# Optimization experiments

Measured on AMD Instinct MI355X. Metric: run time of the kernel, lower is better.

The kernel has to match this reference:

```python
import jax, jax.numpy as jnp
import numpy as np

N = 150000
E = 1200000
IN_DIM = 64
HID = 64


def setup_inputs() -> dict:
    key = jax.random.key(0)
    k1, k2, k3, k4 = jax.random.split(key, 4)
    obs = jax.random.normal(k1, (N, IN_DIM), dtype=jnp.float32)
    edge_index = jax.random.randint(k2, (2, E), 0, N, dtype=jnp.int64)
    # GCNConv layer params (Glorot-style scale)
    W1 = jax.random.normal(k3, (IN_DIM, HID), dtype=jnp.float32) / jnp.sqrt(IN_DIM)
    b1 = jnp.zeros((HID,), dtype=jnp.float32)
    W2 = jax.random.normal(k4, (HID, 1), dtype=jnp.float32) / jnp.sqrt(HID)
    b2 = jnp.zeros((1,), dtype=jnp.float32)
    return {"obs": obs, "edge_index": edge_index, "W1": W1, "b1": b1, "W2": W2, "b2": b2}


def gcn_conv(x, W, b, src, dst, n):
    # PyG GCNConv: x' = D^{-1/2} (A + I) D^{-1/2} (x W) + b
    x = x @ W  # [N, F_out]
    # degree with self-loops (edge weight 1)
    deg = jax.ops.segment_sum(jnp.ones((src.shape[0],), x.dtype), dst, num_segments=n) + 1.0
    dinv = jax.lax.rsqrt(deg)  # deg >= 1, safe
    norm = dinv[src] * dinv[dst]  # per-edge norm
    msg = x[src] * norm[:, None]  # gather + scale
    agg = jax.ops.segment_sum(msg, dst, num_segments=n)
    agg = agg + x * (dinv * dinv)[:, None]  # self-loop term
    return agg + b


def reference(obs, edge_index, W1, b1, W2, b2):
    src, dst = edge_index[0], edge_index[1]
    h1 = jax.nn.relu(gcn_conv(obs, W1, b1, src, dst, N))
    h2 = jax.nn.relu(gcn_conv(h1, W2, b2, src, dst, N))
    out = h2.reshape(-1, 15)[:, 3:].reshape(-1)
    return out
```

## Files before the change

kernel.cpp:

```cpp
#include <hip/hip_runtime.h>
#include <hip/hip_bf16.h>


#define BK 256
#define NBMAX 640
#define EPB 4096
#define HB 320
#define FCAP 3072

typedef unsigned int uint;
typedef unsigned short ushort;
typedef __attribute__((ext_vector_type(8))) short bf16x8_t;
typedef __attribute__((ext_vector_type(4))) float f32x4_t;

static __device__ __forceinline__ ushort f2bf(float x) {
    uint u = __float_as_uint(x);
    u = (u + 0x7FFFu + ((u >> 16) & 1u)) >> 16;
    return (ushort)u;
}

static __device__ __forceinline__ uint pk2(float a, float b) {
    __hip_bfloat162 h = __float22bfloat162_rn(make_float2(a, b));
    return *(uint*)&h;
}

__global__ __launch_bounds__(256) void k_hist(const int* __restrict__ dst, int E, int nb,
                                              int* __restrict__ hist) {
    __shared__ int h[NBMAX];
    const int t = threadIdx.x, b = blockIdx.x;
    for (int j = t; j < nb; j += 256) h[j] = 0;
    __syncthreads();
    const int e0 = b * EPB, e1 = min(e0 + EPB, E);
    if ((((size_t)dst) & 15) == 0) {
        const int nfull = (e1 - e0) & ~3;
        const int4* d4 = (const int4*)(dst + e0);
        for (int i = t; i < (nfull >> 2); i += 256) {
            int4 d = d4[i];
            atomicAdd(&h[d.x >> 8], 1); atomicAdd(&h[d.y >> 8], 1);
            atomicAdd(&h[d.z >> 8], 1); atomicAdd(&h[d.w >> 8], 1);
        }
        for (int e = e0 + nfull + t; e < e1; e += 256) atomicAdd(&h[dst[e] >> 8], 1);
    } else {
        for (int e = e0 + t; e < e1; e += 256) atomicAdd(&h[dst[e] >> 8], 1);
    }
    __syncthreads();
    for (int j = t; j < nb; j += 256) hist[j * HB + b] = h[j];
}

__global__ __launch_bounds__(256) void k_cscan1(int* __restrict__ hist, int nblk,
                                                int* __restrict__ colsum) {
    __shared__ int s[256];
    const int j = blockIdx.x, t = threadIdx.x;
    int carry = 0;
    for (int base = 0; base < nblk; base += 256) {
        int idx = base + t;
        int v = (idx < nblk) ? hist[j * HB + idx] : 0;
        __syncthreads();
        s[t] = v;
        __syncthreads();
        for (int o = 1; o < 256; o <<= 1) {
            int x = s[t];
            if (t >= o) x += s[t - o];
            __syncthreads();
            s[t] = x;
            __syncthreads();
        }
        if (idx < nblk) hist[j * HB + idx] = carry + s[t] - v;
        carry += s[255];
    }
    if (t == 0) colsum[j] = carry;
}

__global__ __launch_bounds__(1024) void k_cscan2(const int* __restrict__ colsum, int nb, int N,
                                                 int* __restrict__ boff, int* __restrict__ rowptr) {
    __shared__ int s[1024];
    const int t = threadIdx.x;
    int v = (t < nb) ? colsum[t] : 0;
    s[t] = v;
    __syncthreads();
    for (int o = 1; o < 1024; o <<= 1) {
        int x = s[t];
        if (t >= o) x += s[t - o];
        __syncthreads();
        s[t] = x;
        __syncthreads();
    }
    if (t < nb) boff[t] = s[t] - v;
    if (t == nb - 1) { boff[nb] = s[t]; rowptr[N] = s[t]; }
}

__global__ __launch_bounds__(256) void k_place(const int* __restrict__ src, const int* __restrict__ dst,
                                               int E, int nb, const int* __restrict__ hist,
                                               const int* __restrict__ boff, uint* __restrict__ ebuf) {
    __shared__ int cur[NBMAX];
    const int t = threadIdx.x, b = blockIdx.x;
    for (int j = t; j < nb; j += 256) cur[j] = boff[j] + hist[j * HB + b];
    __syncthreads();
    const int e0 = b * EPB, e1 = min(e0 + EPB, E);
    if (((((size_t)dst) | ((size_t)src)) & 15) == 0) {
        const int nfull = (e1 - e0) & ~3;
        const int4* d4 = (const int4*)(dst + e0);
        const int4* s4 = (const int4*)(src + e0);
        for (int i = t; i < (nfull >> 2); i += 256) {
            int4 d = d4[i];
            int4 s = s4[i];
            int p;
            p = atomicAdd(&cur[d.x >> 8], 1); ebuf[p] = ((uint)(d.x & 255) << 24) | (uint)s.x;
            p = atomicAdd(&cur[d.y >> 8], 1); ebuf[p] = ((uint)(d.y & 255) << 24) | (uint)s.y;
            p = atomicAdd(&cur[d.z >> 8], 1); ebuf[p] = ((uint)(d.z & 255) << 24) | (uint)s.z;
            p = atomicAdd(&cur[d.w >> 8], 1); ebuf[p] = ((uint)(d.w & 255) << 24) | (uint)s.w;
        }
        for (int e = e0 + nfull + t; e < e1; e += 256) {
            int d = dst[e];
            int p = atomicAdd(&cur[d >> 8], 1);
            ebuf[p] = ((uint)(d & 255) << 24) | (uint)src[e];
        }
    } else {
        for (int e = e0 + t; e < e1; e += 256) {
            int d = dst[e];
            int p = atomicAdd(&cur[d >> 8], 1);
            ebuf[p] = ((uint)(d & 255) << 24) | (uint)src[e];
        }
    }
}

__global__ __launch_bounds__(256) void k_fill3(const uint* __restrict__ ebuf, const int* __restrict__ boff,
                                               int N, int* __restrict__ rowptr, float* __restrict__ dinv,
                                               int* __restrict__ csrc) {
    __shared__ int cnt[BK];
    __shared__ int sc[BK];
    __shared__ int cur[BK];
    __shared__ uint se[FCAP];
    const int b = blockIdx.x, v0 = b << 8, t = threadIdx.x;
    const int nv = min(BK, N - v0);
    cnt[t] = 0;
    __syncthreads();
    const int bb = boff[b], be = boff[b + 1];
    const int ne = be - bb;
    for (int j = t; j < ne; j += 256) {
        uint e = ebuf[bb + j];
        if (j < FCAP) se[j] = e;
        atomicAdd(&cnt[e >> 24], 1);
    }
    __syncthreads();
    const int c = cnt[t];
    if (t < nv) dinv[v0 + t] = rsqrtf((float)c + 1.0f);
    sc[t] = c;
    __syncthreads();
    for (int o = 1; o < 256; o <<= 1) {
        int x = sc[t];
        if (t >= o) x += sc[t - o];
        __syncthreads();
        sc[t] = x;
        __syncthreads();
    }
    const int ex = sc[t] - c + bb;
    if (t < nv) rowptr[v0 + t] = ex;
    cur[t] = ex;
    __syncthreads();
    for (int j = t; j < ne; j += 256) {
        uint e = (j < FCAP) ? se[j] : ebuf[bb + j];
        int p = atomicAdd(&cur[e >> 24], 1);
        csrc[p] = (int)(e & 0xFFFFFFu);
    }
}

__global__ __launch_bounds__(256) void k_gemm1(const float* __restrict__ X, const float* __restrict__ W,
                                               const float* __restrict__ dinv, int N,
                                               ushort* __restrict__ Yh) {
    __shared__ __align__(16) ushort Wt[64 * 72];
    __shared__ __align__(16) ushort Ot[64 * 72];
    const int t = threadIdx.x;

#pragma unroll
    for (int i = 0; i < 4; i++) {
        int idx = t + i * 256;
        int k = idx >> 4;
        int c4 = idx & 15;
        float4 w4 = ((const float4*)W)[idx];
        Wt[(c4 * 4 + 0) * 72 + k] = f2bf(w4.x);
        Wt[(c4 * 4 + 1) * 72 + k] = f2bf(w4.y);
        Wt[(c4 * 4 + 2) * 72 + k] = f2bf(w4.z);
        Wt[(c4 * 4 + 3) * 72 + k] = f2bf(w4.w);
    }
    __syncthreads();

    const int l = t & 63;
    const int lr = l & 15;
    const int g = l >> 4;
    const int wv = t >> 6;

#pragma unroll
    for (int tile = 0; tile < 2; tile++) {
        const int row0 = blockIdx.x * 128 + tile * 64;
        const int rw = row0 + wv * 16;

        bf16x8_t afr[2];
#pragma unroll
        for (int s = 0; s < 2; s++) {
            const int row = rw + lr;
            float4 xa = make_float4(0.f, 0.f, 0.f, 0.f), xb = xa;
            if (row < N) {
                const float4* xp = (const float4*)(X + (size_t)row * 64 + s * 32 + g * 8);
                xa = xp[0];
                xb = xp[1];
            }
            uint4 ua;
            ua.x = pk2(xa.x, xa.y);
            ua.y = pk2(xa.z, xa.w);
            ua.z = pk2(xb.x, xb.y);
            ua.w = pk2(xb.z, xb.w);
            afr[s] = __builtin_bit_cast(bf16x8_t, ua);
        }

        const float4 dv = *(const float4*)(dinv + rw + g * 4);

#pragma unroll
        for (int c = 0; c < 4; c++) {
            f32x4_t acc = {0.f, 0.f, 0.f, 0.f};
#pragma unroll
            for (int s = 0; s < 2; s++) {
                const bf16x8_t bf = *(const bf16x8_t*)&Wt[(c * 16 + lr) * 72 + s * 32 + g * 8];
                acc = __builtin_amdgcn_mfma_f32_16x16x32_bf16(afr[s], bf, acc, 0, 0, 0);
            }
            const int col = c * 16 + lr;
            const int rb = wv * 16 + g * 4;
            uint u01 = pk2(acc[0] * dv.x, acc[1] * dv.y);
            uint u23 = pk2(acc[2] * dv.z, acc[3] * dv.w);
            Ot[(rb + 0) * 72 + col] = (ushort)(u01 & 0xFFFFu);
            Ot[(rb + 1) * 72 + col] = (ushort)(u01 >> 16);
            Ot[(rb + 2) * 72 + col] = (ushort)(u23 & 0xFFFFu);
            Ot[(rb + 3) * 72 + col] = (ushort)(u23 >> 16);
        }
        __syncthreads();

#pragma unroll
        for (int i = 0; i < 2; i++) {
            int vi = t + i * 256;
            int row = vi >> 3;
            int c8 = vi & 7;
            int grow = row0 + row;
            if (grow < N)
                ((uint4*)(Yh + (size_t)grow * 64))[c8] = *(const uint4*)&Ot[row * 72 + c8 * 8];
        }
        __syncthreads();
    }
}

__global__ __launch_bounds__(256) void k_agg(const ushort* __restrict__ Yh, const int* __restrict__ rowptr,
                                             const int* __restrict__ csrc, const float* __restrict__ dinv,
                                             const float* __restrict__ b1, const float* __restrict__ W2,
                                             int N, float* __restrict__ zs) {
    int t = blockIdx.x * 256 + threadIdx.x;
    int v = t >> 3;
    if (v >= N) return;
    int li = t & 7;
    const uint4* Y4 = (const uint4*)Yh;
    int start = rowptr[v];
    int cnt = rowptr[v + 1] - start;

    float a[8];
    {
        uint4 m = Y4[(size_t)v * 8 + li];
        a[0] = __uint_as_float(m.x << 16);
        a[1] = __uint_as_float(m.x & 0xFFFF0000u);
        a[2] = __uint_as_float(m.y << 16);
        a[3] = __uint_as_float(m.y & 0xFFFF0000u);
        a[4] = __uint_as_float(m.z << 16);
        a[5] = __uint_as_float(m.z & 0xFFFF0000u);
        a[6] = __uint_as_float(m.w << 16);
        a[7] = __uint_as_float(m.w & 0xFFFF0000u);
    }

    int idx = (li < cnt) ? csrc[start + li] : 0;
    for (int j0 = 0; j0 < cnt; j0 += 8) {
        int rem = cnt - j0;
        int nxt = 0;
        if (li < rem - 8) nxt = csrc[start + j0 + 8 + li];
#pragma unroll
        for (int k = 0; k < 8; k++) {
            if (k < rem) {
                int s = __shfl(idx, k, 8);
                uint4 m = Y4[(size_t)s * 8 + li];
                a[0] += __uint_as_float(m.x << 16);
                a[1] += __uint_as_float(m.x & 0xFFFF0000u);
                a[2] += __uint_as_float(m.y << 16);
                a[3] += __uint_as_float(m.y & 0xFFFF0000u);
                a[4] += __uint_as_float(m.z << 16);
                a[5] += __uint_as_float(m.z & 0xFFFF0000u);
                a[6] += __uint_as_float(m.w << 16);
                a[7] += __uint_as_float(m.w & 0xFFFF0000u);
            }
        }
        idx = nxt;
    }

    float dv = dinv[v];
    float4 ba = ((const float4*)b1)[2 * li], bb = ((const float4*)b1)[2 * li + 1];
    float4 wa = ((const float4*)W2)[2 * li], wb = ((const float4*)W2)[2 * li + 1];
    float p;
    p  = fmaxf(fmaf(dv, a[0], ba.x), 0.f) * wa.x;
    p += fmaxf(fmaf(dv, a[1], ba.y), 0.f) * wa.y;
    p += fmaxf(fmaf(dv, a[2], ba.z), 0.f) * wa.z;
    p += fmaxf(fmaf(dv, a[3], ba.w), 0.f) * wa.w;
    p += fmaxf(fmaf(dv, a[4], bb.x), 0.f) * wb.x;
    p += fmaxf(fmaf(dv, a[5], bb.y), 0.f) * wb.y;
    p += fmaxf(fmaf(dv, a[6], bb.z), 0.f) * wb.z;
    p += fmaxf(fmaf(dv, a[7], bb.w), 0.f) * wb.w;
    p += __shfl_xor(p, 1);
    p += __shfl_xor(p, 2);
    p += __shfl_xor(p, 4);
    if (li == 0) zs[v] = p * dv;
}

__global__ __launch_bounds__(256) void k_out2(const float* __restrict__ zs, const int* __restrict__ rowptr,
                                              const int* __restrict__ csrc, const float* __restrict__ dinv,
                                              const float* __restrict__ b2, int M, float* __restrict__ out) {
    int i = blockIdx.x * 256 + threadIdx.x;
    if (i >= M) return;
    int q = i / 12;
    int c = i - q * 12;
    int v = q * 15 + 3 + c;
    int j = rowptr[v];
    const int end = rowptr[v + 1];
    float s = zs[v];
    for (; j + 4 <= end; j += 4) {
        int i0 = csrc[j], i1 = csrc[j + 1], i2 = csrc[j + 2], i3 = csrc[j + 3];
        s += zs[i0] + zs[i1] + zs[i2] + zs[i3];
    }
    for (; j < end; j++) s += zs[csrc[j]];
    out[i] = fmaxf(fmaf(dinv[v], s, b2[0]), 0.f);
}

extern "C" void kernel_launch(void* const* d_in, const int* in_sizes, int n_in,
                              void* d_out, int out_size, void* d_ws, size_t ws_size,
                              hipStream_t stream) {
    const float* obs = (const float*)d_in[0];
    const int*   ei  = (const int*)d_in[1];
    const float* W1  = (const float*)d_in[2];
    const float* b1  = (const float*)d_in[3];
    const float* W2  = (const float*)d_in[4];
    const float* b2  = (const float*)d_in[5];

    const int N = in_sizes[0] / 64;
    const int E = in_sizes[1] / 2;
    const int M = out_size;
    const int NB = (N + BK - 1) / BK;
    const int NBLK = (E + EPB - 1) / EPB;

    const int* src = ei;
    const int* dst = ei + E;

    ushort* Yh     = (ushort*)d_ws;
    float*  dinv   = (float*)(Yh + (size_t)N * 64);
    float*  zs     = dinv + N;
    int*    rowptr = (int*)(zs + N);
    int*    colsum = rowptr + N + 1;
    int*    boff   = colsum + NBMAX;
    int*    hist   = boff + NBMAX + 1;
    uint*   ebuf   = (uint*)(hist + NBMAX * HB);
    int*    csrc   = (int*)(ebuf + E);

    k_hist  <<<NBLK, 256, 0, stream>>>(dst, E, NB, hist);
    k_cscan1<<<NB, 256, 0, stream>>>(hist, NBLK, colsum);
    k_cscan2<<<1, 1024, 0, stream>>>(colsum, NB, N, boff, rowptr);
    k_place <<<NBLK, 256, 0, stream>>>(src, dst, E, NB, hist, boff, ebuf);
    k_fill3 <<<NB, 256, 0, stream>>>(ebuf, boff, N, rowptr, dinv, csrc);
    k_gemm1 <<<(N + 127) / 128, 256, 0, stream>>>(obs, W1, dinv, N, Yh);
    k_agg   <<<((size_t)N * 8 + 255) / 256, 256, 0, stream>>>(Yh, rowptr, csrc, dinv, b1, W2, N, zs);
    k_out2  <<<(M + 255) / 256, 256, 0, stream>>>(zs, rowptr, csrc, dinv, b2, M, (float*)d_out);
}
```

Baseline: 89.42 us.

## Fuse histogram with GEMM, drop column-scan kernel, move dinv scaling into aggregation

The destination histogram and the first-layer GEMM now run in one launch, split by block index. This works because the GEMM no longer pre-scales rows by dinv. The source-side dinv factor is applied instead inside the aggregation loop, with a per-neighbour dinv gather and an FMA. The single-block k_cscan2 is removed: k_place rescans colsum itself and k_fill3 reduces a colsum prefix, cutting two launches and one serial step. The cost is extra dinv gathers per edge in aggregation and redundant scan work in every place/fill block.

Measured after the change: 90.00 us. About the same (+0.6%).

```diff
diff --git a/kernel.cpp b/kernel.cpp
--- a/kernel.cpp
+++ b/kernel.cpp
@@ -24,153 +24,38 @@
     return *(uint*)&h;
 }
 
-__global__ __launch_bounds__(256) void k_hist(const int* __restrict__ dst, int E, int nb,
-                                              int* __restrict__ hist) {
-    __shared__ int h[NBMAX];
-    const int t = threadIdx.x, b = blockIdx.x;
-    for (int j = t; j < nb; j += 256) h[j] = 0;
-    __syncthreads();
-    const int e0 = b * EPB, e1 = min(e0 + EPB, E);
-    if ((((size_t)dst) & 15) == 0) {
-        const int nfull = (e1 - e0) & ~3;
-        const int4* d4 = (const int4*)(dst + e0);
-        for (int i = t; i < (nfull >> 2); i += 256) {
-            int4 d = d4[i];
-            atomicAdd(&h[d.x >> 8], 1); atomicAdd(&h[d.y >> 8], 1);
-            atomicAdd(&h[d.z >> 8], 1); atomicAdd(&h[d.w >> 8], 1);
-        }
-        for (int e = e0 + nfull + t; e < e1; e += 256) atomicAdd(&h[dst[e] >> 8], 1);
-    } else {
-        for (int e = e0 + t; e < e1; e += 256) atomicAdd(&h[dst[e] >> 8], 1);
-    }
-    __syncthreads();
-    for (int j = t; j < nb; j += 256) hist[j * HB + b] = h[j];
-}
-
-__global__ __launch_bounds__(256) void k_cscan1(int* __restrict__ hist, int nblk,
-                                                int* __restrict__ colsum) {
-    __shared__ int s[256];
-    const int j = blockIdx.x, t = threadIdx.x;
-    int carry = 0;
-    for (int base = 0; base < nblk; base += 256) {
-        int idx = base + t;
-        int v = (idx < nblk) ? hist[j * HB + idx] : 0;
-        __syncthreads();
-        s[t] = v;
-        __syncthreads();
-        for (int o = 1; o < 256; o <<= 1) {
-            int x = s[t];
-            if (t >= o) x += s[t - o];
-            __syncthreads();
-            s[t] = x;
-            __syncthreads();
-        }
-        if (idx < nblk) hist[j * HB + idx] = carry + s[t] - v;
-        carry += s[255];
-    }
-    if (t == 0) colsum[j] = carry;
-}
-
-__global__ __launch_bounds__(1024) void k_cscan2(const int* __restrict__ colsum, int nb, int N,
-                                                 int* __restrict__ boff, int* __restrict__ rowptr) {
-    __shared__ int s[1024];
+__global__ __launch_bounds__(256) void k_hist_gemm(const int* __restrict__ dst, int E, int nb, int nblk,
+                                                   int* __restrict__ hist,
+                                                   const float* __restrict__ X, const float* __restrict__ W,
+                                                   int N, ushort* __restrict__ Yh) {
+    __shared__ __align__(16) ushort smem[64 * 72 * 2];
     const int t = threadIdx.x;
-    int v = (t < nb) ? colsum[t] : 0;
-    s[t] = v;
-    __syncthreads();
-    for (int o = 1; o < 1024; o <<= 1) {
-        int x = s[t];
-        if (t >= o) x += s[t - o];
-        __syncthreads();
-        s[t] = x;
-        __syncthreads();
-    }
-    if (t < nb) boff[t] = s[t] - v;
-    if (t == nb - 1) { boff[nb] = s[t]; rowptr[N] = s[t]; }
-}
-
-__global__ __launch_bounds__(256) void k_place(const int* __restrict__ src, const int* __restrict__ dst,
-                                               int E, int nb, const int* __restrict__ hist,
-                                               const int* __restrict__ boff, uint* __restrict__ ebuf) {
-    __shared__ int cur[NBMAX];
-    const int t = threadIdx.x, b = blockIdx.x;
-    for (int j = t; j < nb; j += 256) cur[j] = boff[j] + hist[j * HB + b];
-    __syncthreads();
-    const int e0 = b * EPB, e1 = min(e0 + EPB, E);
-    if (((((size_t)dst) | ((size_t)src)) & 15) == 0) {
-        const int nfull = (e1 - e0) & ~3;
-        const int4* d4 = (const int4*)(dst + e0);
-        const int4* s4 = (const int4*)(src + e0);
-        for (int i = t; i < (nfull >> 2); i += 256) {
-            int4 d = d4[i];
-            int4 s = s4[i];
-            int p;
-            p = atomicAdd(&cur[d.x >> 8], 1); ebuf[p] = ((uint)(d.x & 255) << 24) | (uint)s.x;
-            p = atomicAdd(&cur[d.y >> 8], 1); ebuf[p] = ((uint)(d.y & 255) << 24) | (uint)s.y;
-            p = atomicAdd(&cur[d.z >> 8], 1); ebuf[p] = ((uint)(d.z & 255) << 24) | (uint)s.z;
-            p = atomicAdd(&cur[d.w >> 8], 1); ebuf[p] = ((uint)(d.w & 255) << 24) | (uint)s.w;
-        }
-        for (int e = e0 + nfull + t; e < e1; e += 256) {
-            int d = dst[e];
-            int p = atomicAdd(&cur[d >> 8], 1);
-            ebuf[p] = ((uint)(d & 255) << 24) | (uint)src[e];
-        }
-    } else {
-        for (int e = e0 + t; e < e1; e += 256) {
-            int d = dst[e];
-            int p = atomicAdd(&cur[d >> 8], 1);
-            ebuf[p] = ((uint)(d & 255) << 24) | (uint)src[e];
-        }
-    }
-}
-
-__global__ __launch_bounds__(256) void k_fill3(const uint* __restrict__ ebuf, const int* __restrict__ boff,
-                                               int N, int* __restrict__ rowptr, float* __restrict__ dinv,
-                                               int* __restrict__ csrc) {
-    __shared__ int cnt[BK];
-    __shared__ int sc[BK];
-    __shared__ int cur[BK];
-    __shared__ uint se[FCAP];
-    const int b = blockIdx.x, v0 = b << 8, t = threadIdx.x;
-    const int nv = min(BK, N - v0);
-    cnt[t] = 0;
-    __syncthreads();
-    const int bb = boff[b], be = boff[b + 1];
-    const int ne = be - bb;
-    for (int j = t; j < ne; j += 256) {
-        uint e = ebuf[bb + j];
-        if (j < FCAP) se[j] = e;
-        atomicAdd(&cnt[e >> 24], 1);
-    }
-    __syncthreads();
-    const int c = cnt[t];
-    if (t < nv) dinv[v0 + t] = rsqrtf((float)c + 1.0f);
-    sc[t] = c;
-    __syncthreads();
-    for (int o = 1; o < 256; o <<= 1) {
-        int x = sc[t];
-        if (t >= o) x += sc[t - o];
-        __syncthreads();
-        sc[t] = x;
-        __syncthreads();
-    }
-    const int ex = sc[t] - c + bb;
-    if (t < nv) rowptr[v0 + t] = ex;
-    cur[t] = ex;
-    __syncthreads();
-    for (int j = t; j < ne; j += 256) {
-        uint e = (j < FCAP) ? se[j] : ebuf[bb + j];
-        int p = atomicAdd(&cur[e >> 24], 1);
-        csrc[p] = (int)(e & 0xFFFFFFu);
-    }
-}
-
-__global__ __launch_bounds__(256) void k_gemm1(const float* __restrict__ X, const float* __restrict__ W,
-                                               const float* __restrict__ dinv, int N,
-                                               ushort* __restrict__ Yh) {
-    __shared__ __align__(16) ushort Wt[64 * 72];
-    __shared__ __align__(16) ushort Ot[64 * 72];
-    const int t = threadIdx.x;
+
+    if (blockIdx.x < (uint)nblk) {
+        int* h = (int*)smem;
+        const int b = blockIdx.x;
+        for (int j = t; j < nb; j += 256) h[j] = 0;
+        __syncthreads();
+        const int e0 = b * EPB, e1 = min(e0 + EPB, E);
+        if ((((size_t)dst) & 15) == 0) {
+            const int nfull = (e1 - e0) & ~3;
+            const int4* d4 = (const int4*)(dst + e0);
+            for (int i = t; i < (nfull >> 2); i += 256) {
+                int4 d = d4[i];
+                atomicAdd(&h[d.x >> 8], 1); atomicAdd(&h[d.y >> 8], 1);
+                atomicAdd(&h[d.z >> 8], 1); atomicAdd(&h[d.w >> 8], 1);
+            }
+            for (int e = e0 + nfull + t; e < e1; e += 256) atomicAdd(&h[dst[e] >> 8], 1);
+        } else {
+            for (int e = e0 + t; e < e1; e += 256) atomicAdd(&h[dst[e] >> 8], 1);
+        }
+        __syncthreads();
+        for (int j = t; j < nb; j += 256) hist[j * HB + b] = h[j];
+        return;
+    }
+
+    ushort* Wt = smem;
+    ushort* Ot = smem + 64 * 72;
 
 #pragma unroll
     for (int i = 0; i < 4; i++) {
@@ -189,10 +74,11 @@
     const int lr = l & 15;
     const int g = l >> 4;
     const int wv = t >> 6;
+    const int gb = blockIdx.x - nblk;
 
 #pragma unroll
     for (int tile = 0; tile < 2; tile++) {
-        const int row0 = blockIdx.x * 128 + tile * 64;
+        const int row0 = gb * 128 + tile * 64;
         const int rw = row0 + wv * 16;
 
         bf16x8_t afr[2];
@@ -213,8 +99,6 @@
             afr[s] = __builtin_bit_cast(bf16x8_t, ua);
         }
 
-        const float4 dv = *(const float4*)(dinv + rw + g * 4);
-
 #pragma unroll
         for (int c = 0; c < 4; c++) {
             f32x4_t acc = {0.f, 0.f, 0.f, 0.f};
@@ -225,8 +109,8 @@
             }
             const int col = c * 16 + lr;
             const int rb = wv * 16 + g * 4;
-            uint u01 = pk2(acc[0] * dv.x, acc[1] * dv.y);
-            uint u23 = pk2(acc[2] * dv.z, acc[3] * dv.w);
+            uint u01 = pk2(acc[0], acc[1]);
+            uint u23 = pk2(acc[2], acc[3]);
             Ot[(rb + 0) * 72 + col] = (ushort)(u01 & 0xFFFFu);
             Ot[(rb + 1) * 72 + col] = (ushort)(u01 >> 16);
             Ot[(rb + 2) * 72 + col] = (ushort)(u23 & 0xFFFFu);
@@ -244,6 +128,136 @@
                 ((uint4*)(Yh + (size_t)grow * 64))[c8] = *(const uint4*)&Ot[row * 72 + c8 * 8];
         }
         __syncthreads();
+    }
+}
+
+__global__ __launch_bounds__(256) void k_cscan1(int* __restrict__ hist, int nblk,
+                                                int* __restrict__ colsum) {
+    __shared__ int s[256];
+    const int j = blockIdx.x, t = threadIdx.x;
+    int carry = 0;
+    for (int base = 0; base < nblk; base += 256) {
+        int idx = base + t;
+        int v = (idx < nblk) ? hist[j * HB + idx] : 0;
+        __syncthreads();
+        s[t] = v;
+        __syncthreads();
+        for (int o = 1; o < 256; o <<= 1) {
+            int x = s[t];
+            if (t >= o) x += s[t - o];
+            __syncthreads();
+            s[t] = x;
+            __syncthreads();
+        }
+        if (idx < nblk) hist[j * HB + idx] = carry + s[t] - v;
+        carry += s[255];
+    }
+    if (t == 0) colsum[j] = carry;
+}
+
+__global__ __launch_bounds__(256) void k_place(const int* __restrict__ src, const int* __restrict__ dst,
+                                               int E, int nb, const int* __restrict__ hist,
+                                               const int* __restrict__ colsum, uint* __restrict__ ebuf) {
+    __shared__ int cur[NBMAX];
+    __shared__ int s[256];
+    const int t = threadIdx.x, b = blockIdx.x;
+
+    int carry = 0;
+    for (int base = 0; base < nb; base += 256) {
+        int idx = base + t;
+        int v = (idx < nb) ? colsum[idx] : 0;
+        __syncthreads();
+        s[t] = v;
+        __syncthreads();
+        for (int o = 1; o < 256; o <<= 1) {
+            int x = s[t];
+            if (t >= o) x += s[t - o];
+            __syncthreads();
+            s[t] = x;
+            __syncthreads();
+        }
+        if (idx < nb) cur[idx] = carry + s[t] - v + hist[idx * HB + b];
+        carry += s[255];
+    }
+    __syncthreads();
+
+    const int e0 = b * EPB, e1 = min(e0 + EPB, E);
+    if (((((size_t)dst) | ((size_t)src)) & 15) == 0) {
+        const int nfull = (e1 - e0) & ~3;
+        const int4* d4 = (const int4*)(dst + e0);
+        const int4* s4 = (const int4*)(src + e0);
+        for (int i = t; i < (nfull >> 2); i += 256) {
+            int4 d = d4[i];
+            int4 sv = s4[i];
+            int p;
+            p = atomicAdd(&cur[d.x >> 8], 1); ebuf[p] = ((uint)(d.x & 255) << 24) | (uint)sv.x;
+            p = atomicAdd(&cur[d.y >> 8], 1); ebuf[p] = ((uint)(d.y & 255) << 24) | (uint)sv.y;
+            p = atomicAdd(&cur[d.z >> 8], 1); ebuf[p] = ((uint)(d.z & 255) << 24) | (uint)sv.z;
+            p = atomicAdd(&cur[d.w >> 8], 1); ebuf[p] = ((uint)(d.w & 255) << 24) | (uint)sv.w;
+        }
+        for (int e = e0 + nfull + t; e < e1; e += 256) {
+            int d = dst[e];
+            int p = atomicAdd(&cur[d >> 8], 1);
+            ebuf[p] = ((uint)(d & 255) << 24) | (uint)src[e];
+        }
+    } else {
+        for (int e = e0 + t; e < e1; e += 256) {
+            int d = dst[e];
+            int p = atomicAdd(&cur[d >> 8], 1);
+            ebuf[p] = ((uint)(d & 255) << 24) | (uint)src[e];
+        }
+    }
+}
+
+__global__ __launch_bounds__(256) void k_fill3(const uint* __restrict__ ebuf, const int* __restrict__ colsum,
+                                               int N, int E, int* __restrict__ rowptr,
+                                               float* __restrict__ dinv, int* __restrict__ csrc) {
+    __shared__ int cnt[BK];
+    __shared__ int sc[BK];
+    __shared__ int cur[BK];
+    __shared__ int red[256];
+    __shared__ uint se[FCAP];
+    const int b = blockIdx.x, v0 = b << 8, t = threadIdx.x;
+    const int nv = min(BK, N - v0);
+
+    int acc = 0;
+    for (int j = t; j < b; j += 256) acc += colsum[j];
+    red[t] = acc;
+    cnt[t] = 0;
+    __syncthreads();
+    for (int o = 128; o > 0; o >>= 1) {
+        if (t < o) red[t] += red[t + o];
+        __syncthreads();
+    }
+    const int bb = red[0];
+    const int ne = colsum[b];
+    if (b == 0 && t == 0) rowptr[N] = E;
+
+    for (int j = t; j < ne; j += 256) {
+        uint e = ebuf[bb + j];
+        if (j < FCAP) se[j] = e;
+        atomicAdd(&cnt[e >> 24], 1);
+    }
+    __syncthreads();
+    const int c = cnt[t];
+    if (t < nv) dinv[v0 + t] = rsqrtf((float)c + 1.0f);
+    sc[t] = c;
+    __syncthreads();
+    for (int o = 1; o < 256; o <<= 1) {
+        int x = sc[t];
+        if (t >= o) x += sc[t - o];
+        __syncthreads();
+        sc[t] = x;
+        __syncthreads();
+    }
+    const int ex = sc[t] - c + bb;
+    if (t < nv) rowptr[v0 + t] = ex;
+    cur[t] = ex;
+    __syncthreads();
+    for (int j = t; j < ne; j += 256) {
+        uint e = (j < FCAP) ? se[j] : ebuf[bb + j];
+        int p = atomicAdd(&cur[e >> 24], 1);
+        csrc[p] = (int)(e & 0xFFFFFFu);
     }
 }
 
@@ -258,59 +272,64 @@
     const uint4* Y4 = (const uint4*)Yh;
     int start = rowptr[v];
     int cnt = rowptr[v + 1] - start;
+    float dvv = dinv[v];
 
     float a[8];
     {
         uint4 m = Y4[(size_t)v * 8 + li];
-        a[0] = __uint_as_float(m.x << 16);
-        a[1] = __uint_as_float(m.x & 0xFFFF0000u);
-        a[2] = __uint_as_float(m.y << 16);
-        a[3] = __uint_as_float(m.y & 0xFFFF0000u);
-        a[4] = __uint_as_float(m.z << 16);
-        a[5] = __uint_as_float(m.z & 0xFFFF0000u);
-        a[6] = __uint_as_float(m.w << 16);
-        a[7] = __uint_as_float(m.w & 0xFFFF0000u);
-    }
-
-    int idx = (li < cnt) ? csrc[start + li] : 0;
+        a[0] = dvv * __uint_as_float(m.x << 16);
+        a[1] = dvv * __uint_as_float(m.x & 0xFFFF0000u);
+        a[2] = dvv * __uint_as_float(m.y << 16);
+        a[3] = dvv * __uint_as_float(m.y & 0xFFFF0000u);
+        a[4] = dvv * __uint_as_float(m.z << 16);
+        a[5] = dvv * __uint_as_float(m.z & 0xFFFF0000u);
+        a[6] = dvv * __uint_as_float(m.w << 16);
+        a[7] = dvv * __uint_as_float(m.w & 0xFFFF0000u);
+    }
+
+    int idx = 0;
+    float dvl = 0.f;
+    if (li < cnt) { idx = csrc[start + li]; dvl = dinv[idx]; }
     for (int j0 = 0; j0 < cnt; j0 += 8) {
         int rem = cnt - j0;
         int nxt = 0;
-        if (li < rem - 8) nxt = csrc[start + j0 + 8 + li];
+        float ndv = 0.f;
+        if (li < rem - 8) { nxt = csrc[start + j0 + 8 + li]; ndv = dinv[nxt]; }
 #pragma unroll
         for (int k = 0; k < 8; k++) {
             if (k < rem) {
                 int s = __shfl(idx, k, 8);
+                float ds = __shfl(dvl, k, 8);
                 uint4 m = Y4[(size_t)s * 8 + li];
-                a[0] += __uint_as_float(m.x << 16);
-                a[1] += __uint_as_float(m.x & 0xFFFF0000u);
-                a[2] += __uint_as_float(m.y << 16);
-                a[3] += __uint_as_float(m.y & 0xFFFF0000u);
-                a[4] += __uint_as_float(m.z << 16);
-                a[5] += __uint_as_float(m.z & 0xFFFF0000u);
-                a[6] += __uint_as_float(m.w << 16);
-                a[7] += __uint_as_float(m.w & 0xFFFF0000u);
+                a[0] = fmaf(ds, __uint_as_float(m.x << 16), a[0]);
+                a[1] = fmaf(ds, __uint_as_float(m.x & 0xFFFF0000u), a[1]);
+                a[2] = fmaf(ds, __uint_as_float(m.y << 16), a[2]);
+                a[3] = fmaf(ds, __uint_as_float(m.y & 0xFFFF0000u), a[3]);
+                a[4] = fmaf(ds, __uint_as_float(m.z << 16), a[4]);
+                a[5] = fmaf(ds, __uint_as_float(m.z & 0xFFFF0000u), a[5]);
+                a[6] = fmaf(ds, __uint_as_float(m.w << 16), a[6]);
+                a[7] = fmaf(ds, __uint_as_float(m.w & 0xFFFF0000u), a[7]);
             }
         }
         idx = nxt;
-    }
-
-    float dv = dinv[v];
+        dvl = ndv;
+    }
+
     float4 ba = ((const float4*)b1)[2 * li], bb = ((const float4*)b1)[2 * li + 1];
     float4 wa = ((const float4*)W2)[2 * li], wb = ((const float4*)W2)[2 * li + 1];
     float p;
-    p  = fmaxf(fmaf(dv, a[0], ba.x), 0.f) * wa.x;
-    p += fmaxf(fmaf(dv, a[1], ba.y), 0.f) * wa.y;
-    p += fmaxf(fmaf(dv, a[2], ba.z), 0.f) * wa.z;
-    p += fmaxf(fmaf(dv, a[3], ba.w), 0.f) * wa.w;
-    p += fmaxf(fmaf(dv, a[4], bb.x), 0.f) * wb.x;
-    p += fmaxf(fmaf(dv, a[5], bb.y), 0.f) * wb.y;
-    p += fmaxf(fmaf(dv, a[6], bb.z), 0.f) * wb.z;
-    p += fmaxf(fmaf(dv, a[7], bb.w), 0.f) * wb.w;
+    p  = fmaxf(fmaf(dvv, a[0], ba.x), 0.f) * wa.x;
+    p += fmaxf(fmaf(dvv, a[1], ba.y), 0.f) * wa.y;
+    p += fmaxf(fmaf(dvv, a[2], ba.z), 0.f) * wa.z;
+    p += fmaxf(fmaf(dvv, a[3], ba.w), 0.f) * wa.w;
+    p += fmaxf(fmaf(dvv, a[4], bb.x), 0.f) * wb.x;
+    p += fmaxf(fmaf(dvv, a[5], bb.y), 0.f) * wb.y;
+    p += fmaxf(fmaf(dvv, a[6], bb.z), 0.f) * wb.z;
+    p += fmaxf(fmaf(dvv, a[7], bb.w), 0.f) * wb.w;
     p += __shfl_xor(p, 1);
     p += __shfl_xor(p, 2);
     p += __shfl_xor(p, 4);
-    if (li == 0) zs[v] = p * dv;
+    if (li == 0) zs[v] = p * dvv;
 }
 
 __global__ __launch_bounds__(256) void k_out2(const float* __restrict__ zs, const int* __restrict__ rowptr,
@@ -347,6 +366,7 @@
     const int M = out_size;
     const int NB = (N + BK - 1) / BK;
     const int NBLK = (E + EPB - 1) / EPB;
+    const int GEMMB = (N + 127) / 128;
 
     const int* src = ei;
     const int* dst = ei + E;
@@ -356,17 +376,14 @@
     float*  zs     = dinv + N;
     int*    rowptr = (int*)(zs + N);
     int*    colsum = rowptr + N + 1;
-    int*    boff   = colsum + NBMAX;
-    int*    hist   = boff + NBMAX + 1;
+    int*    hist   = colsum + NBMAX;
     uint*   ebuf   = (uint*)(hist + NBMAX * HB);
     int*    csrc   = (int*)(ebuf + E);
 
-    k_hist  <<<NBLK, 256, 0, stream>>>(dst, E, NB, hist);
-    k_cscan1<<<NB, 256, 0, stream>>>(hist, NBLK, colsum);
-    k_cscan2<<<1, 1024, 0, stream>>>(colsum, NB, N, boff, rowptr);
-    k_place <<<NBLK, 256, 0, stream>>>(src, dst, E, NB, hist, boff, ebuf);
-    k_fill3 <<<NB, 256, 0, stream>>>(ebuf, boff, N, rowptr, dinv, csrc);
-    k_gemm1 <<<(N + 127) / 128, 256, 0, stream>>>(obs, W1, dinv, N, Yh);
-    k_agg   <<<((size_t)N * 8 + 255) / 256, 256, 0, stream>>>(Yh, rowptr, csrc, dinv, b1, W2, N, zs);
-    k_out2  <<<(M + 255) / 256, 256, 0, stream>>>(zs, rowptr, csrc, dinv, b2, M, (float*)d_out);
-}
+    k_hist_gemm<<<NBLK + GEMMB, 256, 0, stream>>>(dst, E, NB, NBLK, hist, obs, W1, N, Yh);
+    k_cscan1   <<<NB, 256, 0, stream>>>(hist, NBLK, colsum);
+    k_place    <<<NBLK, 256, 0, stream>>>(src, dst, E, NB, hist, colsum, ebuf);
+    k_fill3    <<<NB, 256, 0, stream>>>(ebuf, colsum, N, E, rowptr, dinv, csrc);
+    k_agg      <<<((size_t)N * 8 + 255) / 256, 256, 0, stream>>>(Yh, rowptr, csrc, dinv, b1, W2, N, zs);
+    k_out2     <<<(M + 255) / 256, 256, 0, stream>>>(zs, rowptr, csrc, dinv, b2, M, (float*)d_out);
+}
```
